# Performance work log

Hardware: AMD Instinct MI355X
Metric: run time of the kernel (lower is better)

## Reference

```python
import jax, jax.numpy as jnp
import numpy as np

B, DIN, H = 16384, 512, 512
K = 7  # LC_i1, LC_i2, LC_f1, LC_f2, LC_o, LC_z (gate nets, idx 0..5), LC_d (decay net, idx 6)


def setup_inputs() -> dict:
    key = jax.random.key(0)
    ks = jax.random.split(key, 8)
    s1 = 1.0 / np.sqrt(DIN)
    s2 = 1.0 / np.sqrt(H)
    return {
        "hx": jax.random.normal(ks[0], (B, DIN), jnp.float32),
        "cx1": jax.random.normal(ks[1], (B, H), jnp.float32),
        "cx2": jax.random.normal(ks[2], (B, H), jnp.float32),
        # stacked params for the 7 sub-networks (same structure: Linear(DIN,H) -> Linear(H,H))
        "W1": jax.random.uniform(ks[3], (K, H, DIN), jnp.float32, -s1, s1),
        "b1": jax.random.uniform(ks[4], (K, H), jnp.float32, -s1, s1),
        "W2": jax.random.uniform(ks[5], (K, H, H), jnp.float32, -s2, s2),
        "b2": jax.random.uniform(ks[6], (K, H), jnp.float32, -s2, s2),
    }


def reference(hx, cx1, cx2, W1, b1, W2, b2):
    # layer 1 for all 7 nets at once: [K, B, H]
    h1 = jnp.einsum('bd,khd->kbh', hx, W1) + b1[:, None, :]
    # gate nets use tanh, decay net uses softplus
    a1 = jnp.concatenate([jnp.tanh(h1[:6]), jax.nn.softplus(h1[6:])], axis=0)
    # layer 2: [K, B, H]
    h2 = jnp.einsum('kbh,kgh->kbg', a1, W2) + b2[:, None, :]
    gates = jax.nn.sigmoid(jnp.tanh(h2[:6]))  # Gate_network: sigmoid(tanh(.))
    d = jax.nn.softplus(h2[6])                # Decay_network output (decay_coef, side state)
    i1, i2, f1, f2, o, zg = gates
    z = jnp.tanh(zg)                          # z = Tanh(LC_z(hx))
    cy1 = f1 * cx1 + i1 * z                   # side state self.cy1
    cy2 = f2 * cx2 + i2 * z
    return cy2
```

## Files before the change

### kernel.cpp

```cpp
#include <hip/hip_runtime.h>
#include <hip/hip_bf16.h>

typedef __attribute__((ext_vector_type(8))) __bf16 bf16x8;
typedef __attribute__((ext_vector_type(4))) __bf16 bf16x4;
typedef __attribute__((ext_vector_type(4))) float f32x4;

constexpr int M = 16384;
constexpr int K = 512;
constexpr int BK = 32;
constexpr int NT = 16;

__device__ __forceinline__ void async_copy16(const void* gsrc, void* ldst) {
  __builtin_amdgcn_global_load_lds(
      (const __attribute__((address_space(1))) unsigned int*)(gsrc),
      (__attribute__((address_space(3))) unsigned int*)(ldst),
      16, 0, 0);
}

__device__ __forceinline__ float frcp(float x) { return __builtin_amdgcn_rcpf(x); }
__device__ __forceinline__ float ftanh(float x) {
  return 1.0f - 2.0f * frcp(1.0f + __expf(2.0f * x));
}
__device__ __forceinline__ float fsigm(float x) { return frcp(1.0f + __expf(-x)); }

__device__ __forceinline__ int kswz(int row) {
  return ((row & 3) << 3) ^ ((row & 12) << 2);
}

template <int MODE>
__global__ __launch_bounds__(256)
__attribute__((amdgpu_waves_per_eu(2))) void gemm_kernel(
    const __bf16* __restrict__ Ab,
    const __bf16* __restrict__ W,
    const float* __restrict__ bias,
    __bf16* __restrict__ outb)
{
  const int jj = blockIdx.z;
  const int mbase = blockIdx.x * 256;
  const int nbase = blockIdx.y * 128;
  constexpr size_t NH = (size_t)M * 512;

  const __bf16* Aj = (MODE == 1) ? Ab : Ab + (size_t)jj * NH;
  const __bf16* Wj = W + (size_t)jj * 262144;
  const int brow = 2 * jj + 1;

  __shared__ __align__(16) __bf16 smem[36864];

  const int tid  = threadIdx.x;
  const int wid  = tid >> 6;
  const int lane = tid & 63;
  const int wm   = (wid >> 1) * 128;
  const int wn   = (wid & 1) * 64;
  const int srow = wid * 16 + (lane >> 2);
  const int scol = ((lane & 3) ^ ((lane >> 3) & 3)) * 8;
  const int fr   = lane & 15;
  const int kc   = lane >> 4;
  const int sw   = (fr >> 1) & 3;
  const int rowq = kc * 4;

  auto stage = [&](int p, int k0) {
    __bf16* As = smem + p * 12288;
    __bf16* Bs = As + 8192;
#pragma unroll
    for (int r = 0; r < 4; ++r)
      async_copy16(Aj + (size_t)(mbase + r * 64 + srow) * K + (k0 + scol),
                   (void*)&As[(r * 64 + wid * 16) * BK]);
#pragma unroll
    for (int r = 0; r < 2; ++r)
      async_copy16(Wj + (size_t)(nbase + r * 64 + srow) * K + (k0 + scol),
                   (void*)&Bs[(r * 64 + wid * 16) * BK]);
  };

  f32x4 acc[8][4] = {};

  stage(0, 0);
  stage(1, BK);
  int pr = 0, ps = 2;
  for (int t = 0; t < NT; ++t) {
    if (t < NT - 2) asm volatile("s_waitcnt vmcnt(6) lgkmcnt(0)" ::: "memory");
    else            asm volatile("s_waitcnt vmcnt(0) lgkmcnt(0)" ::: "memory");
    __builtin_amdgcn_s_barrier();
    __builtin_amdgcn_sched_barrier(0);
    if (t < NT - 2) stage(ps, (t + 2) * BK);

    const __bf16* As = smem + pr * 12288;
    const __bf16* Bs = As + 8192;
    bf16x8 af[8], bfr[4];
#pragma unroll
    for (int i = 0; i < 8; ++i)
      af[i]  = *(const bf16x8*)&As[(wm + i * 16 + fr) * BK + ((kc ^ sw) * 8)];
#pragma unroll
    for (int i = 0; i < 4; ++i)
      bfr[i] = *(const bf16x8*)&Bs[(wn + i * 16 + fr) * BK + ((kc ^ sw) * 8)];
#pragma unroll
    for (int mi = 0; mi < 8; ++mi)
#pragma unroll
      for (int ni = 0; ni < 4; ++ni)
        acc[mi][ni] = __builtin_amdgcn_mfma_f32_16x16x32_bf16(
            af[mi], bfr[ni], acc[mi][ni], 0, 0, 0);

    pr = (pr == 2) ? 0 : pr + 1;
    ps = (ps == 2) ? 0 : ps + 1;
  }

  float bv[4];
  const float* bj = bias + (size_t)brow * 512 + nbase + wn;
#pragma unroll
  for (int ni = 0; ni < 4; ++ni) bv[ni] = bj[ni * 16 + fr];

  __syncthreads();
#pragma unroll
  for (int mi = 0; mi < 8; ++mi)
#pragma unroll
    for (int ni = 0; ni < 4; ++ni)
#pragma unroll
      for (int r = 0; r < 4; ++r) {
        float v = acc[mi][ni][r] + bv[ni];
        float res;
        if constexpr (MODE == 1) res = ftanh(v);
        else res = (jj == 2) ? ftanh(fsigm(ftanh(v)))
                             : fsigm(ftanh(v));
        const int row = wm + mi * 16 + rowq + r;
        const int col = wn + ni * 16 + fr;
        smem[row * 128 + (col ^ kswz(row))] = (__bf16)res;
      }
  __syncthreads();
#pragma unroll
  for (int it = 0; it < 16; ++it) {
    const int s = it * 256 + tid;
    const int row = s >> 4, ch = s & 15;
    bf16x8 v = *(const bf16x8*)&smem[row * 128 + ((ch * 8) ^ kswz(row))];
    *(bf16x8*)&outb[(size_t)jj * NH + (size_t)(mbase + row) * 512 +
                    (nbase + ch * 8)] = v;
  }
}

__global__ __launch_bounds__(256) void final_kernel(
    const __bf16* __restrict__ gates, const float* __restrict__ cx2,
    float* __restrict__ out)
{
  constexpr size_t NH = (size_t)M * 512;
  const size_t i = ((size_t)blockIdx.x * 256 + threadIdx.x) * 8;
  bf16x8 i2 = *(const bf16x8*)&gates[i];
  bf16x8 f2 = *(const bf16x8*)&gates[NH + i];
  bf16x8 zz = *(const bf16x8*)&gates[2 * NH + i];
  f32x4 c0 = *(const f32x4*)&cx2[i];
  f32x4 c1 = *(const f32x4*)&cx2[i + 4];
#pragma unroll
  for (int h = 0; h < 2; ++h) {
    f32x4 r;
#pragma unroll
    for (int q = 0; q < 4; ++q) {
      const int e = h * 4 + q;
      r[q] = (float)f2[e] * (h ? c1[q] : c0[q]) + (float)i2[e] * (float)zz[e];
    }
    *(f32x4*)&out[i + h * 4] = r;
  }
}

__global__ __launch_bounds__(256) void cvt_all(const float* __restrict__ hx,
                                               const float* __restrict__ W1,
                                               const float* __restrict__ W2,
                                               __bf16* __restrict__ hxb,
                                               __bf16* __restrict__ Wb) {
  const int b = blockIdx.x;
  if (b < 1536) {
    const int y = b >> 8;
    const int bb = b & 255;
    const float* src = (y < 3) ? W1 + (size_t)(2 * y + 1) * 262144
                               : W2 + (size_t)(2 * (y - 3) + 1) * 262144;
    __bf16* d = Wb + (size_t)y * 262144;
    const size_t i = ((size_t)bb * 256 + threadIdx.x) * 4;
    f32x4 v = *(const f32x4*)&src[i];
    *(bf16x4*)&d[i] = __builtin_convertvector(v, bf16x4);
  } else {
    const size_t i = ((size_t)(b - 1536) * 256 + threadIdx.x) * 4;
    f32x4 v = *(const f32x4*)&hx[i];
    *(bf16x4*)&hxb[i] = __builtin_convertvector(v, bf16x4);
  }
}

extern "C" void kernel_launch(void* const* d_in, const int* in_sizes, int n_in,
                              void* d_out, int out_size, void* d_ws, size_t ws_size,
                              hipStream_t stream) {
  const float* hx  = (const float*)d_in[0];
  const float* cx2 = (const float*)d_in[2];
  const float* W1  = (const float*)d_in[3];
  const float* b1  = (const float*)d_in[4];
  const float* W2  = (const float*)d_in[5];
  const float* b2  = (const float*)d_in[6];
  float* out = (float*)d_out;

  char* ws = (char*)d_ws;
  __bf16* Wb    = (__bf16*)(ws);
  __bf16* hxb   = (__bf16*)(ws + 3145728);
  __bf16* a1    = (__bf16*)(ws + 19922944);
  __bf16* gates = (__bf16*)(ws + 70254592);
  __bf16* W2b   = Wb + 3 * 262144;

  cvt_all<<<9728, 256, 0, stream>>>(hx, W1, W2, hxb, Wb);

  gemm_kernel<1><<<dim3(64, 4, 3), 256, 0, stream>>>(hxb, Wb, b1, a1);
  gemm_kernel<2><<<dim3(64, 4, 3), 256, 0, stream>>>(a1, W2b, b2, gates);
  final_kernel<<<4096, 256, 0, stream>>>(gates, cx2, out);
}
```

Before: 233.7 us.

## Restructure GEMM into 8-wave 256x256 tiles with interleaved load/MFMA phases

Replaces the 4-wave 256x128 GEMM with an 8-wave 512-thread kernel computing 256x256 tiles at BK=64 with double-buffered LDS. The K-loop is split into four quadrant phases that interleave LDS fragment loads, async global prefetch and MFMA bursts, with barriers and s_setprio between them. The aim is to raise arithmetic intensity per block and hide memory latency behind MFMA work. In exchange it uses 128KB of LDS per block, launches half as many blocks (384), and adds more barriers per iteration. The epilogue is staged in two halves to fit the wider tile.

```diff
diff --git a/kernel.cpp b/kernel.cpp
--- a/kernel.cpp
+++ b/kernel.cpp
@@ -7,8 +7,8 @@
 
 constexpr int M = 16384;
 constexpr int K = 512;
-constexpr int BK = 32;
-constexpr int NT = 16;
+constexpr int BKT = 64;
+constexpr int NKT = 8;
 
 __device__ __forceinline__ void async_copy16(const void* gsrc, void* ldst) {
   __builtin_amdgcn_global_load_lds(
@@ -27,9 +27,23 @@
   return ((row & 3) << 3) ^ ((row & 12) << 2);
 }
 
+#define MIDSYNC                                                  \
+  __builtin_amdgcn_s_barrier();                                  \
+  asm volatile("s_waitcnt lgkmcnt(0)" ::: "memory");             \
+  __builtin_amdgcn_sched_barrier(0);
+#define ENDSYNC                                                  \
+  __builtin_amdgcn_s_barrier();                                  \
+  __builtin_amdgcn_sched_barrier(0);
+
+#define QUAD(g, p, AF, BF)                                               \
+  _Pragma("unroll") for (int i_ = 0; i_ < 4; ++i_)                       \
+  _Pragma("unroll") for (int n_ = 0; n_ < 2; ++n_)                       \
+  _Pragma("unroll") for (int kk_ = 0; kk_ < 2; ++kk_)                    \
+    acc[(g)*4 + i_][(p)*2 + n_] = __builtin_amdgcn_mfma_f32_16x16x32_bf16( \
+        AF[i_][kk_], BF[n_][kk_], acc[(g)*4 + i_][(p)*2 + n_], 0, 0, 0);
+
 template <int MODE>
-__global__ __launch_bounds__(256)
-__attribute__((amdgpu_waves_per_eu(2))) void gemm_kernel(
+__global__ __launch_bounds__(512, 2) void gemm8(
     const __bf16* __restrict__ Ab,
     const __bf16* __restrict__ W,
     const float* __restrict__ bias,
@@ -37,70 +51,106 @@
 {
   const int jj = blockIdx.z;
   const int mbase = blockIdx.x * 256;
-  const int nbase = blockIdx.y * 128;
+  const int nbase = blockIdx.y * 256;
   constexpr size_t NH = (size_t)M * 512;
-
   const __bf16* Aj = (MODE == 1) ? Ab : Ab + (size_t)jj * NH;
   const __bf16* Wj = W + (size_t)jj * 262144;
   const int brow = 2 * jj + 1;
 
-  __shared__ __align__(16) __bf16 smem[36864];
-
-  const int tid  = threadIdx.x;
-  const int wid  = tid >> 6;
-  const int lane = tid & 63;
-  const int wm   = (wid >> 1) * 128;
-  const int wn   = (wid & 1) * 64;
-  const int srow = wid * 16 + (lane >> 2);
-  const int scol = ((lane & 3) ^ ((lane >> 3) & 3)) * 8;
-  const int fr   = lane & 15;
-  const int kc   = lane >> 4;
-  const int sw   = (fr >> 1) & 3;
+  __shared__ __align__(16) __bf16 smem[65536];
+
+  const int tid = threadIdx.x, wid = tid >> 6, lane = tid & 63;
+  const int a  = wid & 1;
+  const int wn = (wid >> 1) * 64;
+  const int b  = wid >> 2;
+  const int fr = lane & 15, kc = lane >> 4;
   const int rowq = kc * 4;
 
-  auto stage = [&](int p, int k0) {
-    __bf16* As = smem + p * 12288;
-    __bf16* Bs = As + 8192;
-#pragma unroll
-    for (int r = 0; r < 4; ++r)
-      async_copy16(Aj + (size_t)(mbase + r * 64 + srow) * K + (k0 + scol),
-                   (void*)&As[(r * 64 + wid * 16) * BK]);
-#pragma unroll
-    for (int r = 0; r < 2; ++r)
-      async_copy16(Wj + (size_t)(nbase + r * 64 + srow) * K + (k0 + scol),
-                   (void*)&Bs[(r * 64 + wid * 16) * BK]);
+  const int sr8 = lane >> 3;
+  const int sch = (lane & 7) ^ sr8;
+  const int w1 = wid >> 1;
+  const int w2 = wid & 3;
+  const __bf16* Asrc =
+      Aj + (size_t)(mbase + a * 128 + w1 * 32 + sr8) * K + sch * 8;
+  const __bf16* Bsrc =
+      Wj + (size_t)(nbase + b * 128 + w2 * 32 + sr8) * K + sch * 8;
+  const int AdstB = a * 8192 + w1 * 32 * 64;
+  const int BdstB = 16384 + b * 8192 + w2 * 32 * 64;
+
+  auto stageA = [&](int beta, int k0) {
+#pragma unroll
+    for (int c = 0; c < 4; ++c)
+      async_copy16(Asrc + (size_t)(c * 8) * K + k0,
+                   (void*)&smem[beta * 32768 + AdstB + c * 512]);
+  };
+  auto stageB = [&](int beta, int k0) {
+#pragma unroll
+    for (int c = 0; c < 4; ++c)
+      async_copy16(Bsrc + (size_t)(c * 8) * K + k0,
+                   (void*)&smem[beta * 32768 + BdstB + c * 512]);
+  };
+
+  auto ldA = [&](int beta, int g, bf16x8 (&af)[4][2]) {
+#pragma unroll
+    for (int i = 0; i < 4; ++i)
+#pragma unroll
+      for (int kk = 0; kk < 2; ++kk) {
+        const int r = (g * 4 + i) * 16 + fr;
+        af[i][kk] = *(const bf16x8*)&smem[beta * 32768 + a * 8192 + r * 64 +
+                                          (((kk << 2) | kc) ^ (fr & 7)) * 8];
+      }
+  };
+  auto ldB = [&](int beta, int p, bf16x8 (&bf)[2][2]) {
+#pragma unroll
+    for (int n = 0; n < 2; ++n)
+#pragma unroll
+      for (int kk = 0; kk < 2; ++kk) {
+        const int r = (wn & 64) + (p * 2 + n) * 16 + fr;
+        bf[n][kk] = *(const bf16x8*)&smem[beta * 32768 + 16384 + b * 8192 +
+                                          r * 64 +
+                                          (((kk << 2) | kc) ^ (fr & 7)) * 8];
+      }
   };
 
   f32x4 acc[8][4] = {};
 
-  stage(0, 0);
-  stage(1, BK);
-  int pr = 0, ps = 2;
-  for (int t = 0; t < NT; ++t) {
-    if (t < NT - 2) asm volatile("s_waitcnt vmcnt(6) lgkmcnt(0)" ::: "memory");
-    else            asm volatile("s_waitcnt vmcnt(0) lgkmcnt(0)" ::: "memory");
-    __builtin_amdgcn_s_barrier();
-    __builtin_amdgcn_sched_barrier(0);
-    if (t < NT - 2) stage(ps, (t + 2) * BK);
-
-    const __bf16* As = smem + pr * 12288;
-    const __bf16* Bs = As + 8192;
-    bf16x8 af[8], bfr[4];
-#pragma unroll
-    for (int i = 0; i < 8; ++i)
-      af[i]  = *(const bf16x8*)&As[(wm + i * 16 + fr) * BK + ((kc ^ sw) * 8)];
-#pragma unroll
-    for (int i = 0; i < 4; ++i)
-      bfr[i] = *(const bf16x8*)&Bs[(wn + i * 16 + fr) * BK + ((kc ^ sw) * 8)];
-#pragma unroll
-    for (int mi = 0; mi < 8; ++mi)
-#pragma unroll
-      for (int ni = 0; ni < 4; ++ni)
-        acc[mi][ni] = __builtin_amdgcn_mfma_f32_16x16x32_bf16(
-            af[mi], bfr[ni], acc[mi][ni], 0, 0, 0);
-
-    pr = (pr == 2) ? 0 : pr + 1;
-    ps = (ps == 2) ? 0 : ps + 1;
+  stageB(0, 0);    stageA(0, 0);
+  stageB(1, BKT);  stageA(1, BKT);
+  asm volatile("s_waitcnt vmcnt(8)" ::: "memory");
+  __builtin_amdgcn_s_barrier();
+  __builtin_amdgcn_sched_barrier(0);
+
+  bf16x8 afA[4][2], afB[4][2], bfA[2][2], bfB[2][2];
+#pragma unroll 1
+  for (int t = 0; t < NKT; ++t) {
+    const int beta = t & 1;
+    const bool pre = (t + 2 < NKT);
+    ldA(beta, 0, afA);
+    ldB(beta, 0, bfA);
+    MIDSYNC;
+    __builtin_amdgcn_s_setprio(1); QUAD(0, 0, afA, bfA);
+    __builtin_amdgcn_s_setprio(0);
+    ENDSYNC;
+    ldB(beta, 1, bfB);
+    MIDSYNC;
+    __builtin_amdgcn_s_setprio(1); QUAD(0, 1, afA, bfB);
+    __builtin_amdgcn_s_setprio(0);
+    ENDSYNC;
+    ldA(beta, 1, afB);
+    if (pre) stageB(beta, (t + 2) * BKT);
+    MIDSYNC;
+    __builtin_amdgcn_s_setprio(1); QUAD(1, 0, afB, bfA);
+    __builtin_amdgcn_s_setprio(0);
+    ENDSYNC;
+    if (pre) stageA(beta, (t + 2) * BKT);
+    MIDSYNC;
+    __builtin_amdgcn_s_setprio(1); QUAD(1, 1, afB, bfB);
+    __builtin_amdgcn_s_setprio(0);
+    if (t < NKT - 1) {
+      if (pre) asm volatile("s_waitcnt vmcnt(8)" ::: "memory");
+      else     asm volatile("s_waitcnt vmcnt(0)" ::: "memory");
+    }
+    ENDSYNC;
   }
 
   float bv[4];
@@ -110,28 +160,35 @@
 
   __syncthreads();
 #pragma unroll
-  for (int mi = 0; mi < 8; ++mi)
-#pragma unroll
-    for (int ni = 0; ni < 4; ++ni)
-#pragma unroll
-      for (int r = 0; r < 4; ++r) {
-        float v = acc[mi][ni][r] + bv[ni];
-        float res;
-        if constexpr (MODE == 1) res = ftanh(v);
-        else res = (jj == 2) ? ftanh(fsigm(ftanh(v)))
-                             : fsigm(ftanh(v));
-        const int row = wm + mi * 16 + rowq + r;
-        const int col = wn + ni * 16 + fr;
-        smem[row * 128 + (col ^ kswz(row))] = (__bf16)res;
-      }
-  __syncthreads();
-#pragma unroll
-  for (int it = 0; it < 16; ++it) {
-    const int s = it * 256 + tid;
-    const int row = s >> 4, ch = s & 15;
-    bf16x8 v = *(const bf16x8*)&smem[row * 128 + ((ch * 8) ^ kswz(row))];
-    *(bf16x8*)&outb[(size_t)jj * NH + (size_t)(mbase + row) * 512 +
-                    (nbase + ch * 8)] = v;
+  for (int h = 0; h < 2; ++h) {
+    if (a == h) {
+#pragma unroll
+      for (int mi = 0; mi < 8; ++mi)
+#pragma unroll
+        for (int ni = 0; ni < 4; ++ni)
+#pragma unroll
+          for (int r = 0; r < 4; ++r) {
+            float v = acc[mi][ni][r] + bv[ni];
+            float res;
+            if constexpr (MODE == 1) res = ftanh(v);
+            else res = (jj == 2) ? ftanh(fsigm(ftanh(v)))
+                                 : fsigm(ftanh(v));
+            const int row = mi * 16 + rowq + r;
+            const int col = wn + ni * 16 + fr;
+            smem[row * 256 + (col ^ kswz(row))] = (__bf16)res;
+          }
+    }
+    __syncthreads();
+#pragma unroll
+    for (int it = 0; it < 8; ++it) {
+      const int s = it * 512 + tid;
+      const int row = s >> 5, ch = s & 31;
+      bf16x8 v = *(const bf16x8*)&smem[row * 256 + ((ch * 8) ^ kswz(row))];
+      *(bf16x8*)&outb[(size_t)jj * NH +
+                      (size_t)(mbase + h * 128 + row) * 512 + (nbase + ch * 8)] =
+          v;
+    }
+    __syncthreads();
   }
 }
 
@@ -163,10 +220,10 @@
                                                const float* __restrict__ W2,
                                                __bf16* __restrict__ hxb,
                                                __bf16* __restrict__ Wb) {
-  const int b = blockIdx.x;
-  if (b < 1536) {
-    const int y = b >> 8;
-    const int bb = b & 255;
+  const int bk = blockIdx.x;
+  if (bk < 1536) {
+    const int y = bk >> 8;
+    const int bb = bk & 255;
     const float* src = (y < 3) ? W1 + (size_t)(2 * y + 1) * 262144
                                : W2 + (size_t)(2 * (y - 3) + 1) * 262144;
     __bf16* d = Wb + (size_t)y * 262144;
@@ -174,7 +231,7 @@
     f32x4 v = *(const f32x4*)&src[i];
     *(bf16x4*)&d[i] = __builtin_convertvector(v, bf16x4);
   } else {
-    const size_t i = ((size_t)(b - 1536) * 256 + threadIdx.x) * 4;
+    const size_t i = ((size_t)(bk - 1536) * 256 + threadIdx.x) * 4;
     f32x4 v = *(const f32x4*)&hx[i];
     *(bf16x4*)&hxb[i] = __builtin_convertvector(v, bf16x4);
   }
@@ -200,7 +257,7 @@
 
   cvt_all<<<9728, 256, 0, stream>>>(hx, W1, W2, hxb, Wb);
 
-  gemm_kernel<1><<<dim3(64, 4, 3), 256, 0, stream>>>(hxb, Wb, b1, a1);
-  gemm_kernel<2><<<dim3(64, 4, 3), 256, 0, stream>>>(a1, W2b, b2, gates);
+  gemm8<1><<<dim3(64, 2, 3), 512, 0, stream>>>(hxb, Wb, b1, a1);
+  gemm8<2><<<dim3(64, 2, 3), 512, 0, stream>>>(a1, W2b, b2, gates);
   final_kernel<<<4096, 256, 0, stream>>>(gates, cx2, out);
 }
```

New measurement: 281.7 us. 1.21x slower.
